# Kernel tuning notes

Measured on AMD Instinct MI355X. Metric: run time of the kernel, lower is better.

Reference implementation:

```python
import jax, jax.numpy as jnp
import numpy as np

N_NODES = 100000
N_EDGES = 1280000
D_IN = 64
D_HID = 64
D_OUT = 64


def sage_conv(x, src, dst, W_l, b_l, W_r):
    # PyG SAGEConv (aggr='mean', root_weight=True):
    #   out_i = W_l @ mean_{j in N(i)} x_j + b_l + W_r @ x_i
    msg = x[src]  # [E, d] gather of source-node features
    agg = jax.ops.segment_sum(msg, dst, num_segments=N_NODES)
    cnt = jax.ops.segment_sum(jnp.ones((src.shape[0],), x.dtype), dst,
                              num_segments=N_NODES)
    mean = agg / jnp.maximum(cnt, 1.0)[:, None]
    return mean @ W_l.T + b_l + x @ W_r.T


def setup_inputs() -> dict:
    key = jax.random.key(0)
    ks = jax.random.split(key, 8)
    x = jax.random.normal(ks[0], (N_NODES, D_IN), dtype=jnp.float32)
    edge_index = jax.random.randint(ks[1], (2, N_EDGES), 0, N_NODES,
                                    dtype=jnp.int64)
    s1 = 1.0 / np.sqrt(D_IN)
    s2 = 1.0 / np.sqrt(D_HID)
    W1_l = jax.random.uniform(ks[2], (D_HID, D_IN), jnp.float32, -s1, s1)
    b1 = jnp.zeros((D_HID,), jnp.float32)
    W1_r = jax.random.uniform(ks[3], (D_HID, D_IN), jnp.float32, -s1, s1)
    W2_l = jax.random.uniform(ks[4], (D_OUT, D_HID), jnp.float32, -s2, s2)
    b2 = jnp.zeros((D_OUT,), jnp.float32)
    W2_r = jax.random.uniform(ks[5], (D_OUT, D_HID), jnp.float32, -s2, s2)
    return {"x": x, "edge_index": edge_index,
            "W1_l": W1_l, "b1": b1, "W1_r": W1_r,
            "W2_l": W2_l, "b2": b2, "W2_r": W2_r}


def reference(x, edge_index, W1_l, b1, W1_r, W2_l, b2, W2_r):
    src, dst = edge_index[0], edge_index[1]
    h = sage_conv(x, src, dst, W1_l, b1, W1_r)
    h = jax.nn.relu(h)
    # dropout p=0.0 -> identity
    out = sage_conv(h, src, dst, W2_l, b2, W2_r)
    return out
```

## Files before the change

kernel.cpp:

```cpp
#include <hip/hip_runtime.h>

#define NN 100000
#define NE 1280000
#define D  64

#define BINSZ   512
#define NBIN    196
#define ESTRIDE 7168
#define CHUNK   4096
#define NT      (NN / 16)

typedef unsigned int   uint;
typedef unsigned short ushort;
typedef unsigned char  uchar;
typedef __attribute__((ext_vector_type(8))) short short8v;
typedef __attribute__((ext_vector_type(4))) float f32x4;

__device__ __forceinline__ ushort f2bf(float f) {
    uint u = __float_as_uint(f);
    uint r = (u + 0x7fffu + ((u >> 16) & 1u)) >> 16;
    return (ushort)r;
}
__device__ __forceinline__ float bf2f(ushort h) {
    return __uint_as_float(((uint)h) << 16);
}
__device__ __forceinline__ float bfhi_f(uint w) { return __uint_as_float(w & 0xffff0000u); }
__device__ __forceinline__ float bflo_f(uint w) { return __uint_as_float(w << 16); }
__device__ __forceinline__ uint packbf(float a, float b) {
    return (uint)f2bf(a) | ((uint)f2bf(b) << 16);
}

#define XBLKS 3125
__global__ __launch_bounds__(256) void prep(const float* __restrict__ x,
                                            uint* __restrict__ xb,
                                            const float* __restrict__ w0,
                                            const float* __restrict__ w1,
                                            const float* __restrict__ w2,
                                            const float* __restrict__ w3,
                                            ushort* __restrict__ hi,
                                            ushort* __restrict__ lo) {
    const int bid = blockIdx.x;
    if (bid < XBLKS) {
        const int g = bid * 256 + threadIdx.x;
        const float4* xp = (const float4*)x + (size_t)g * 2;
        const float4 v0 = xp[0], v1 = xp[1];
        uint4 o;
        o.x = packbf(v0.x, v0.y);
        o.y = packbf(v0.z, v0.w);
        o.z = packbf(v1.x, v1.y);
        o.w = packbf(v1.z, v1.w);
        ((uint4*)xb)[g] = o;
    } else {
        const int g = (bid - XBLKS) * 256 + threadIdx.x;
        if (g < 4 * 4096) {
            const int m = g >> 12;
            const float* src = (m == 0) ? w0 : (m == 1) ? w1 : (m == 2) ? w2 : w3;
            const float f = src[g & 4095];
            const ushort h = f2bf(f);
            hi[g] = h;
            lo[g] = f2bf(f - bf2f(h));
        }
    }
}

__global__ __launch_bounds__(256) void bin_scatter(const int* __restrict__ srcv,
                                                   const int* __restrict__ dstv,
                                                   int* __restrict__ bincur,
                                                   uint* __restrict__ ecol) {
    __shared__ uint  ebuf[CHUNK];
    __shared__ uchar bbuf[CHUNK];
    __shared__ int hist[256];
    __shared__ int hbase[256];
    __shared__ int gbase[256];

    const int tid  = threadIdx.x;
    const int base = blockIdx.x * CHUNK;

    hist[tid] = 0;
    __syncthreads();

    uint pk[16];
    int  bn[16], rk[16];
    #pragma unroll
    for (int r = 0; r < 16; ++r) {
        const int e = base + r * 256 + tid;
        if (e < NE) {
            const int d = dstv[e];
            bn[r] = d >> 9;
            pk[r] = ((uint)srcv[e] << 9) | (uint)(d & 511);
            rk[r] = atomicAdd(&hist[bn[r]], 1);
        } else {
            bn[r] = -1;
        }
    }
    __syncthreads();

    const int v = hist[tid];
    hbase[tid] = v;
    __syncthreads();
    for (int d = 1; d < 256; d <<= 1) {
        const int t = (tid >= d) ? hbase[tid - d] : 0;
        __syncthreads();
        hbase[tid] += t;
        __syncthreads();
    }
    hbase[tid] -= v;
    if (tid < NBIN && v > 0)
        gbase[tid] = atomicAdd(&bincur[tid], v);
    __syncthreads();

    #pragma unroll
    for (int r = 0; r < 16; ++r) {
        if (bn[r] >= 0) {
            const int p = hbase[bn[r]] + rk[r];
            ebuf[p] = pk[r];
            bbuf[p] = (uchar)bn[r];
        }
    }
    __syncthreads();

    const int n = min(CHUNK, NE - base);
    for (int i = tid; i < n; i += 256) {
        const int b   = bbuf[i];
        const int pib = gbase[b] + (i - hbase[b]);
        if (pib < ESTRIDE)
            ecol[(size_t)b * ESTRIDE + pib] = ebuf[i];
    }
}

__global__ __launch_bounds__(1024) void binsort(const uint* __restrict__ ecol,
                                                const int* __restrict__ bincur,
                                                int* __restrict__ col,
                                                int* __restrict__ offs) {
    __shared__ int hist[512];
    __shared__ int cnt_[512];
    __shared__ int gdst_s;

    const int b = blockIdx.x;
    const int t = threadIdx.x;
    const int n    = min(bincur[b], ESTRIDE);
    const int gsrc = b * ESTRIDE;

    if (t < 512) hist[t] = 0;
    if (t < 64) {
        int s = 0;
        for (int i = t; i < b; i += 64) s += min(bincur[i], ESTRIDE);
        #pragma unroll
        for (int d = 1; d < 64; d <<= 1) s += __shfl_xor(s, d);
        if (t == 0) gdst_s = s;
    }
    __syncthreads();
    const int gdst = gdst_s;

    const int NIT = ESTRIDE / 1024;
    int nd[NIT], ee[NIT], rk[NIT];
    #pragma unroll
    for (int it = 0; it < NIT; ++it) {
        const int i = t + it * 1024;
        if (i < n) {
            const uint e = ecol[gsrc + i];
            nd[it] = (int)(e & 511);
            ee[it] = (int)(e >> 9);
            rk[it] = atomicAdd(&hist[nd[it]], 1);
        } else {
            nd[it] = -1;
        }
    }
    __syncthreads();

    int v = 0;
    if (t < 512) { v = hist[t]; cnt_[t] = v; }
    __syncthreads();
    for (int d = 1; d < 512; d <<= 1) {
        const int tv = (t >= d && t < 512) ? hist[t - d] : 0;
        __syncthreads();
        if (t < 512) hist[t] += tv;
        __syncthreads();
    }
    if (t < 512) {
        const int excl = hist[t] - cnt_[t];
        hist[t] = excl;
        const int node = b * BINSZ + t;
        if (node < NN) offs[node] = gdst + excl;
        if (b == NBIN - 1 && node == NN - 1) offs[NN] = gdst + n;
    }
    __syncthreads();

    #pragma unroll
    for (int it = 0; it < NIT; ++it)
        if (nd[it] >= 0)
            col[gdst + hist[nd[it]] + rk[it]] = ee[it];
}

__device__ __forceinline__ void gload(int (&id)[4], uint4 (&r0)[4], uint4 (&r1)[4],
                                      int k0, int deg, const int* __restrict__ col,
                                      int o0, const uint* __restrict__ gsrc, int q) {
    #pragma unroll
    for (int u = 0; u < 4; ++u) {
        const int k = k0 + u;
        id[u] = (k < deg) ? __builtin_nontemporal_load(col + o0 + k) : -1;
    }
    #pragma unroll
    for (int u = 0; u < 4; ++u) {
        if (id[u] >= 0) {
            const uint* row = gsrc + (size_t)id[u] * 32;
            r0[u] = *(const uint4*)(row + 4 * q);
            r1[u] = *(const uint4*)(row + 16 + 4 * q);
        }
    }
}

__device__ __forceinline__ void gconsume(const int (&id)[4], const uint4 (&r0)[4],
                                         const uint4 (&r1)[4], float (&acc)[16]) {
    #pragma unroll
    for (int u = 0; u < 4; ++u) {
        if (id[u] >= 0) {
            uint w;
            w = r0[u].x; acc[0]  += bflo_f(w); acc[1]  += bfhi_f(w);
            w = r0[u].y; acc[2]  += bflo_f(w); acc[3]  += bfhi_f(w);
            w = r0[u].z; acc[4]  += bflo_f(w); acc[5]  += bfhi_f(w);
            w = r0[u].w; acc[6]  += bflo_f(w); acc[7]  += bfhi_f(w);
            w = r1[u].x; acc[8]  += bflo_f(w); acc[9]  += bfhi_f(w);
            w = r1[u].y; acc[10] += bflo_f(w); acc[11] += bfhi_f(w);
            w = r1[u].z; acc[12] += bflo_f(w); acc[13] += bfhi_f(w);
            w = r1[u].w; acc[14] += bflo_f(w); acc[15] += bfhi_f(w);
        }
    }
}

template<int SELF_BF16, int WF32, int WB16>
__global__ __launch_bounds__(256) void fused_layer(
        const uint*   __restrict__ gsrc,
        const float*  __restrict__ selff,
        const ushort* __restrict__ selfb,
        const int*    __restrict__ col,
        const int*    __restrict__ offs,
        const ushort* __restrict__ wl_hi, const ushort* __restrict__ wl_lo,
        const ushort* __restrict__ wr_hi, const ushort* __restrict__ wr_lo,
        const float*  __restrict__ bias,
        float* __restrict__ outf, ushort* __restrict__ outb,
        int do_relu)
{
    const int l   = threadIdx.x & 63;
    const int wid = (blockIdx.x * 256 + threadIdx.x) >> 6;
    if (wid >= NT) return;
    const int m16   = l & 15;
    const int q     = l >> 4;
    const int koff  = q * 8;
    const int mbase = wid * 16;
    const int node  = mbase + m16;

    const int o0  = offs[node];
    const int deg = offs[node + 1] - o0;

    float acc[16];
    #pragma unroll
    for (int j = 0; j < 16; ++j) acc[j] = 0.f;

    int idA[4], idB[4];
    uint4 a0[4], a1[4], b0[4], b1[4];

    if (__any(deg > 0)) {
        gload(idA, a0, a1, 0, deg, col, o0, gsrc, q);
        int k = 4;
        for (;;) {
            const bool more = __any(k < deg);
            if (more) gload(idB, b0, b1, k, deg, col, o0, gsrc, q);
            gconsume(idA, a0, a1, acc);
            if (!more) break;
            k += 4;
            const bool more2 = __any(k < deg);
            if (more2) gload(idA, a0, a1, k, deg, col, o0, gsrc, q);
            gconsume(idB, b0, b1, acc);
            if (!more2) break;
            k += 4;
        }
    }

    const float inv = 1.0f / (float)max(deg, 1);
    short8v am[2];
    #pragma unroll
    for (int j = 0; j < 8; ++j) {
        am[0][j] = (short)f2bf(acc[j] * inv);
        am[1][j] = (short)f2bf(acc[8 + j] * inv);
    }

    short8v ashi[2], aslo[2];
    if (SELF_BF16) {
        ashi[0] = *(const short8v*)(selfb + (size_t)node * 64 + koff);
        ashi[1] = *(const short8v*)(selfb + (size_t)node * 64 + 32 + koff);
    } else {
        #pragma unroll
        for (int kk = 0; kk < 2; ++kk) {
            const float4* xp = (const float4*)(selff + (size_t)node * 64 + kk * 32 + koff);
            const float4 v0 = xp[0], v1 = xp[1];
            const float vv[8] = {v0.x, v0.y, v0.z, v0.w, v1.x, v1.y, v1.z, v1.w};
            #pragma unroll
            for (int j = 0; j < 8; ++j) {
                const ushort hb_ = f2bf(vv[j]);
                ashi[kk][j] = (short)hb_;
                aslo[kk][j] = (short)f2bf(vv[j] - bf2f(hb_));
            }
        }
    }

    #pragma unroll
    for (int nt = 0; nt < 4; ++nt) {
        f32x4 acc4 = {0.f, 0.f, 0.f, 0.f};
        #pragma unroll
        for (int kk = 0; kk < 2; ++kk) {
            const size_t wo = (size_t)(nt * 16 + m16) * 64 + kk * 32 + koff;
            const short8v bwlh = *(const short8v*)(wl_hi + wo);
            const short8v bwll = *(const short8v*)(wl_lo + wo);
            const short8v bwrh = *(const short8v*)(wr_hi + wo);
            const short8v bwrl = *(const short8v*)(wr_lo + wo);
            acc4 = __builtin_amdgcn_mfma_f32_16x16x32_bf16(am[kk],   bwlh, acc4, 0, 0, 0);
            acc4 = __builtin_amdgcn_mfma_f32_16x16x32_bf16(am[kk],   bwll, acc4, 0, 0, 0);
            acc4 = __builtin_amdgcn_mfma_f32_16x16x32_bf16(ashi[kk], bwrh, acc4, 0, 0, 0);
            if (!SELF_BF16)
                acc4 = __builtin_amdgcn_mfma_f32_16x16x32_bf16(aslo[kk], bwrh, acc4, 0, 0, 0);
            acc4 = __builtin_amdgcn_mfma_f32_16x16x32_bf16(ashi[kk], bwrl, acc4, 0, 0, 0);
        }
        const float bv = bias[nt * 16 + m16];
        #pragma unroll
        for (int r = 0; r < 4; ++r) {
            float v = acc4[r] + bv;
            if (do_relu) v = fmaxf(v, 0.f);
            const size_t oi = (size_t)(mbase + q * 4 + r) * 64 + nt * 16 + m16;
            if (WF32) __builtin_nontemporal_store(v, &outf[oi]);
            if (WB16) __builtin_nontemporal_store(f2bf(v), &outb[oi]);
        }
    }
}

extern "C" void kernel_launch(void* const* d_in, const int* in_sizes, int n_in,
                              void* d_out, int out_size, void* d_ws, size_t ws_size,
                              hipStream_t stream) {
    const float* x   = (const float*)d_in[0];
    const int*   ei  = (const int*)d_in[1];
    const float* W1l = (const float*)d_in[2];
    const float* b1  = (const float*)d_in[3];
    const float* W1r = (const float*)d_in[4];
    const float* W2l = (const float*)d_in[5];
    const float* b2  = (const float*)d_in[6];
    const float* W2r = (const float*)d_in[7];
    float*       out = (float*)d_out;

    const int* src = ei;
    const int* dst = ei + NE;

    char* p = (char*)d_ws;
    int*    bincur = (int*)p;    p += 1024;
    int*    col    = (int*)p;    p += (size_t)NE * 4;
    int*    offs   = (int*)p;    p += (size_t)(NN + 1) * 4 + 60;
    ushort* whi    = (ushort*)p; p += (size_t)4 * 4096 * 2;
    ushort* wlo    = (ushort*)p; p += (size_t)4 * 4096 * 2;
    uint*   xb     = (uint*)p;   p += (size_t)NN * 32 * 4;
    uint*   hb     = (uint*)p;   p += (size_t)NN * 32 * 4;
    uint*   ecol   = hb;

    const ushort* w1l_hi = whi;             const ushort* w1l_lo = wlo;
    const ushort* w1r_hi = whi + 4096;      const ushort* w1r_lo = wlo + 4096;
    const ushort* w2l_hi = whi + 2 * 4096;  const ushort* w2l_lo = wlo + 2 * 4096;
    const ushort* w2r_hi = whi + 3 * 4096;  const ushort* w2r_lo = wlo + 3 * 4096;

    hipMemsetAsync(bincur, 0, 1024, stream);

    prep<<<XBLKS + 64, 256, 0, stream>>>(x, xb, W1l, W1r, W2l, W2r, whi, wlo);

    bin_scatter<<<(NE + CHUNK - 1) / CHUNK, 256, 0, stream>>>(src, dst, bincur, ecol);
    binsort<<<NBIN, 1024, 0, stream>>>(ecol, bincur, col, offs);

    fused_layer<0, 0, 1><<<(NT * 64 + 255) / 256, 256, 0, stream>>>(
        xb, x, nullptr, col, offs,
        w1l_hi, w1l_lo, w1r_hi, w1r_lo, b1, nullptr, (ushort*)hb, 1);

    fused_layer<1, 1, 0><<<(NT * 64 + 255) / 256, 256, 0, stream>>>(
        hb, nullptr, (const ushort*)hb, col, offs,
        w2l_hi, w2l_lo, w2r_hi, w2r_lo, b2, out, nullptr, 0);
}
```

Before: 257.6 us.

## Merge prep into scatter, shard binsort buckets by source, drop nontemporal hints

Folds the bf16 conversion of x and weights into the bin scatter kernel as extra blocks, removing one launch and letting the two independent jobs share the GPU. Binsort now splits each destination node's bucket into 16 sub-buckets keyed by the high source-id bits and uses a wave-shuffle scan instead of the barrier-heavy Hillis-Steele scan. Edges within a node therefore come out roughly grouped by source id, which should give better cache locality in the gather. Nontemporal loads and stores are replaced with ordinary ones so col and the outputs can stay in cache. In exchange the larger shared histogram costs more shared memory and more zeroing work per block.

After: 244.4 us. -5.1%, faster.

```diff
diff --git a/kernel.cpp b/kernel.cpp
--- a/kernel.cpp
+++ b/kernel.cpp
@@ -9,6 +9,12 @@
 #define ESTRIDE 7168
 #define CHUNK   4096
 #define NT      (NN / 16)
+#define NSHARD  16
+#define NBUCKET (BINSZ * NSHARD)
+
+#define SCATB   ((NE + CHUNK - 1) / CHUNK)
+#define XBLKS   3125
+#define WBLKS   64
 
 typedef unsigned int   uint;
 typedef unsigned short ushort;
@@ -30,51 +36,48 @@
     return (uint)f2bf(a) | ((uint)f2bf(b) << 16);
 }
 
-#define XBLKS 3125
-__global__ __launch_bounds__(256) void prep(const float* __restrict__ x,
-                                            uint* __restrict__ xb,
-                                            const float* __restrict__ w0,
-                                            const float* __restrict__ w1,
-                                            const float* __restrict__ w2,
-                                            const float* __restrict__ w3,
-                                            ushort* __restrict__ hi,
-                                            ushort* __restrict__ lo) {
-    const int bid = blockIdx.x;
-    if (bid < XBLKS) {
-        const int g = bid * 256 + threadIdx.x;
-        const float4* xp = (const float4*)x + (size_t)g * 2;
-        const float4 v0 = xp[0], v1 = xp[1];
-        uint4 o;
-        o.x = packbf(v0.x, v0.y);
-        o.y = packbf(v0.z, v0.w);
-        o.z = packbf(v1.x, v1.y);
-        o.w = packbf(v1.z, v1.w);
-        ((uint4*)xb)[g] = o;
-    } else {
-        const int g = (bid - XBLKS) * 256 + threadIdx.x;
-        if (g < 4 * 4096) {
-            const int m = g >> 12;
-            const float* src = (m == 0) ? w0 : (m == 1) ? w1 : (m == 2) ? w2 : w3;
-            const float f = src[g & 4095];
-            const ushort h = f2bf(f);
-            hi[g] = h;
-            lo[g] = f2bf(f - bf2f(h));
-        }
-    }
-}
-
-__global__ __launch_bounds__(256) void bin_scatter(const int* __restrict__ srcv,
-                                                   const int* __restrict__ dstv,
-                                                   int* __restrict__ bincur,
-                                                   uint* __restrict__ ecol) {
+__global__ __launch_bounds__(256) void scatter_prep(
+        const int* __restrict__ srcv, const int* __restrict__ dstv,
+        int* __restrict__ bincur, uint* __restrict__ ecol,
+        const float* __restrict__ x, uint* __restrict__ xb,
+        const float* __restrict__ w0, const float* __restrict__ w1,
+        const float* __restrict__ w2, const float* __restrict__ w3,
+        ushort* __restrict__ hi, ushort* __restrict__ lo) {
     __shared__ uint  ebuf[CHUNK];
     __shared__ uchar bbuf[CHUNK];
     __shared__ int hist[256];
     __shared__ int hbase[256];
     __shared__ int gbase[256];
 
-    const int tid  = threadIdx.x;
-    const int base = blockIdx.x * CHUNK;
+    const int bid = blockIdx.x;
+    const int tid = threadIdx.x;
+
+    if (bid >= SCATB) {
+        if (bid < SCATB + XBLKS) {
+            const int g = (bid - SCATB) * 256 + tid;
+            const float4* xp = (const float4*)x + (size_t)g * 2;
+            const float4 v0 = xp[0], v1 = xp[1];
+            uint4 o;
+            o.x = packbf(v0.x, v0.y);
+            o.y = packbf(v0.z, v0.w);
+            o.z = packbf(v1.x, v1.y);
+            o.w = packbf(v1.z, v1.w);
+            ((uint4*)xb)[g] = o;
+        } else {
+            const int g = (bid - SCATB - XBLKS) * 256 + tid;
+            if (g < 4 * 4096) {
+                const int m = g >> 12;
+                const float* src = (m == 0) ? w0 : (m == 1) ? w1 : (m == 2) ? w2 : w3;
+                const float f = src[g & 4095];
+                const ushort h = f2bf(f);
+                hi[g] = h;
+                lo[g] = f2bf(f - bf2f(h));
+            }
+        }
+        return;
+    }
+
+    const int base = bid * CHUNK;
 
     hist[tid] = 0;
     __syncthreads();
@@ -132,64 +135,83 @@
                                                 const int* __restrict__ bincur,
                                                 int* __restrict__ col,
                                                 int* __restrict__ offs) {
-    __shared__ int hist[512];
-    __shared__ int cnt_[512];
+    __shared__ int hist[NBUCKET];
+    __shared__ int wpart[16];
     __shared__ int gdst_s;
 
     const int b = blockIdx.x;
     const int t = threadIdx.x;
+    const int lane = t & 63;
+    const int wv   = t >> 6;
     const int n    = min(bincur[b], ESTRIDE);
     const int gsrc = b * ESTRIDE;
 
-    if (t < 512) hist[t] = 0;
-    if (t < 64) {
+    #pragma unroll
+    for (int j = 0; j < NBUCKET / 1024; ++j) hist[t + j * 1024] = 0;
+
+    if (wv == 0) {
         int s = 0;
-        for (int i = t; i < b; i += 64) s += min(bincur[i], ESTRIDE);
+        for (int i = lane; i < b; i += 64) s += min(bincur[i], ESTRIDE);
         #pragma unroll
         for (int d = 1; d < 64; d <<= 1) s += __shfl_xor(s, d);
-        if (t == 0) gdst_s = s;
+        if (lane == 0) gdst_s = s;
     }
     __syncthreads();
     const int gdst = gdst_s;
 
     const int NIT = ESTRIDE / 1024;
-    int nd[NIT], ee[NIT], rk[NIT];
+    int bk[NIT], sv[NIT], rk[NIT];
     #pragma unroll
     for (int it = 0; it < NIT; ++it) {
         const int i = t + it * 1024;
         if (i < n) {
             const uint e = ecol[gsrc + i];
-            nd[it] = (int)(e & 511);
-            ee[it] = (int)(e >> 9);
-            rk[it] = atomicAdd(&hist[nd[it]], 1);
+            bk[it] = (int)(((e & 511u) << 4) | (e >> 22));
+            sv[it] = (int)(e >> 9);
+            rk[it] = atomicAdd(&hist[bk[it]], 1);
         } else {
-            nd[it] = -1;
-        }
-    }
-    __syncthreads();
-
-    int v = 0;
-    if (t < 512) { v = hist[t]; cnt_[t] = v; }
-    __syncthreads();
-    for (int d = 1; d < 512; d <<= 1) {
-        const int tv = (t >= d && t < 512) ? hist[t - d] : 0;
-        __syncthreads();
-        if (t < 512) hist[t] += tv;
-        __syncthreads();
-    }
-    if (t < 512) {
-        const int excl = hist[t] - cnt_[t];
-        hist[t] = excl;
+            bk[it] = -1;
+        }
+    }
+    __syncthreads();
+
+    int own[8], s = 0;
+    #pragma unroll
+    for (int j = 0; j < 8; ++j) { own[j] = hist[t * 8 + j]; s += own[j]; }
+    int incl = s;
+    #pragma unroll
+    for (int d = 1; d < 64; d <<= 1) {
+        const int up = __shfl_up(incl, d);
+        if (lane >= d) incl += up;
+    }
+    if (lane == 63) wpart[wv] = incl;
+    __syncthreads();
+    if (wv == 0) {
+        int p = (lane < 16) ? wpart[lane] : 0;
+        int ip = p;
+        #pragma unroll
+        for (int d = 1; d < 16; d <<= 1) {
+            const int up = __shfl_up(ip, d);
+            if (lane >= d) ip += up;
+        }
+        if (lane < 16) wpart[lane] = ip - p;
+    }
+    __syncthreads();
+    int run = wpart[wv] + incl - s;
+    #pragma unroll
+    for (int j = 0; j < 8; ++j) { const int c = own[j]; hist[t * 8 + j] = run; run += c; }
+    __syncthreads();
+
+    if (t < BINSZ) {
         const int node = b * BINSZ + t;
-        if (node < NN) offs[node] = gdst + excl;
+        if (node < NN) offs[node] = gdst + hist[t * 16];
         if (b == NBIN - 1 && node == NN - 1) offs[NN] = gdst + n;
     }
-    __syncthreads();
 
     #pragma unroll
     for (int it = 0; it < NIT; ++it)
-        if (nd[it] >= 0)
-            col[gdst + hist[nd[it]] + rk[it]] = ee[it];
+        if (bk[it] >= 0)
+            col[gdst + hist[bk[it]] + rk[it]] = sv[it];
 }
 
 __device__ __forceinline__ void gload(int (&id)[4], uint4 (&r0)[4], uint4 (&r1)[4],
@@ -198,7 +220,7 @@
     #pragma unroll
     for (int u = 0; u < 4; ++u) {
         const int k = k0 + u;
-        id[u] = (k < deg) ? __builtin_nontemporal_load(col + o0 + k) : -1;
+        id[u] = (k < deg) ? col[o0 + k] : -1;
     }
     #pragma unroll
     for (int u = 0; u < 4; ++u) {
@@ -327,8 +349,8 @@
             float v = acc4[r] + bv;
             if (do_relu) v = fmaxf(v, 0.f);
             const size_t oi = (size_t)(mbase + q * 4 + r) * 64 + nt * 16 + m16;
-            if (WF32) __builtin_nontemporal_store(v, &outf[oi]);
-            if (WB16) __builtin_nontemporal_store(f2bf(v), &outb[oi]);
+            if (WF32) outf[oi] = v;
+            if (WB16) outb[oi] = f2bf(v);
         }
     }
 }
@@ -366,9 +388,9 @@
 
     hipMemsetAsync(bincur, 0, 1024, stream);
 
-    prep<<<XBLKS + 64, 256, 0, stream>>>(x, xb, W1l, W1r, W2l, W2r, whi, wlo);
-
-    bin_scatter<<<(NE + CHUNK - 1) / CHUNK, 256, 0, stream>>>(src, dst, bincur, ecol);
+    scatter_prep<<<SCATB + XBLKS + WBLKS, 256, 0, stream>>>(
+        src, dst, bincur, ecol, x, xb, W1l, W1r, W2l, W2r, whi, wlo);
+
     binsort<<<NBIN, 1024, 0, stream>>>(ecol, bincur, col, offs);
 
     fused_layer<0, 0, 1><<<(NT * 64 + 255) / 256, 256, 0, stream>>>(
```
